# Kernel optimization log

Hardware: AMD Instinct MI355X
Metric: run time of the kernel (lower is better)

The kernel has to match this reference:

```python
import jax, jax.numpy as jnp
import numpy as np
from jax import lax

HIDDEN = 256      # hidden_dim
LATENT = 128      # latent_dim
VOCAB = 32000     # vocab_size
MAX_LEN = 64      # max_len (stack capacity guard, as in original)
MAX_STEPS = 128   # fixed step budget for the decode stack machine
N_NODES = 511     # complete binary tree, depth 9


def _linear_params(key, fan_in, fan_out):
    k1, k2 = jax.random.split(key)
    s = 1.0 / np.sqrt(fan_in)
    W = jax.random.uniform(k1, (fan_out, fan_in), minval=-s, maxval=s, dtype=jnp.float32)
    b = jax.random.uniform(k2, (fan_out,), minval=-s, maxval=s, dtype=jnp.float32)
    return W, b


def setup_inputs() -> dict:
    key = jax.random.key(0)
    ks = jax.random.split(key, 10)
    embed = jax.random.normal(ks[0], (VOCAB, HIDDEN), dtype=jnp.float32)
    Wpar, bpar = _linear_params(ks[1], 3 * HIDDEN, HIDDEN)
    Wmu, bmu = _linear_params(ks[2], HIDDEN, LATENT)
    Wlv, blv = _linear_params(ks[3], HIDDEN, LATENT)
    W1, b1 = _linear_params(ks[4], LATENT, HIDDEN)
    W2, b2 = _linear_params(ks[5], HIDDEN, HIDDEN + 1)
    Wl, bl = _linear_params(ks[6], HIDDEN, VOCAB)
    Wp, bp = _linear_params(ks[7], HIDDEN, 2 * LATENT + VOCAB)
    values = jax.random.randint(ks[8], (N_NODES,), 0, VOCAB)
    idx = np.arange(N_NODES)
    left = np.where(2 * idx + 1 < N_NODES, 2 * idx + 1, -1).astype(np.int32)
    right = np.where(2 * idx + 2 < N_NODES, 2 * idx + 2, -1).astype(np.int32)
    eps = jax.random.normal(ks[9], (LATENT,), dtype=jnp.float32)
    return dict(embed=embed, Wpar=Wpar, bpar=bpar, Wmu=Wmu, bmu=bmu,
                Wlv=Wlv, blv=blv, W1=W1, b1=b1, W2=W2, b2=b2,
                Wl=Wl, bl=bl, Wp=Wp, bp=bp, eps=eps,
                values=jnp.asarray(values), left=jnp.asarray(left), right=jnp.asarray(right))


def reference(embed, Wpar, bpar, Wmu, bmu, Wlv, blv, W1, b1, W2, b2,
              Wl, bl, Wp, bp, eps, values, left, right):
    # ---------- encode: bottom-up over tree stored as index arrays ----------
    emb = embed[values]  # [N, H], one gather for all node embeddings

    def enc_step(h, i):
        v = emb[i]
        li = jnp.maximum(left[i], 0)
        ri = jnp.maximum(right[i], 0)
        cat = jnp.concatenate([v, h[li], h[ri]])          # [3H]
        hp = cat @ Wpar.T + bpar                           # parent combine
        hi = jnp.where(left[i] < 0, v, hp)                 # leaf -> embedding
        return h.at[i].set(hi), None

    h0 = jnp.zeros((values.shape[0], HIDDEN), dtype=embed.dtype)
    # children have larger index than parents -> process in descending order
    h, _ = lax.scan(enc_step, h0, jnp.arange(values.shape[0] - 1, -1, -1))
    root = h[0]
    mu = root @ Wmu.T + bmu
    logvar = root @ Wlv.T + blv
    z = mu + eps * jnp.exp(0.5 * logvar)                   # reparameterize

    # ---------- decode: stack machine with fixed step budget ----------
    V, L = VOCAB, LATENT
    stack0 = jnp.zeros((MAX_LEN, L), dtype=z.dtype).at[0].set(z)
    out0 = jnp.zeros((MAX_STEPS, V), dtype=z.dtype)

    def dec_step(state, _):
        stack, sp, out, op = state
        active = sp > 0
        idx = jnp.maximum(sp - 1, 0)
        node = stack[idx]                                  # pop
        hmid = jax.nn.leaky_relu(node @ W1.T + b1, 0.2)
        co = hmid @ W2.T + b2                              # [H+1]; co[0] = gate
        is_parent = (co[0] > 0) & (sp - 1 <= MAX_LEN - 2) & active

        def parent_fn(_):
            dec = co[1:] @ Wp.T + bp                       # [V + 2L]
            value = dec[:V]
            ll = dec[V:V + L]
            rl = dec[V + L:]
            # original appends llatent then rlatent -> rlatent on top
            st = stack.at[idx].set(ll).at[idx + 1].set(rl)
            return value, st, sp + 1

        def leaf_fn(_):
            return co[1:] @ Wl.T + bl, stack, sp - 1

        value, st, nsp = lax.cond(is_parent, parent_fn, leaf_fn, None)
        m = active.astype(z.dtype)
        out = out.at[op].add(m * value)                    # rows written once
        stack = jnp.where(active, st, stack)
        sp = jnp.where(active, nsp, sp)
        op = op + active.astype(op.dtype)
        return (stack, sp, out, op), None

    init = (stack0, jnp.int32(1), out0, jnp.int32(0))
    (_, _, out, _), _ = lax.scan(dec_step, init, None, length=MAX_STEPS)
    return out, mu, logvar
```

## Files before the change

kernel.cpp:

```cpp
#include <hip/hip_runtime.h>

#define HID 256
#define LAT 128
#define VOC 32000
#define NSTEP 128

__global__ __launch_bounds__(512)
void prep_kernel(const float* __restrict__ Wp, const float* __restrict__ W2,
                 const float* __restrict__ b2, const float* __restrict__ bp,
                 const float* __restrict__ Wpar,
                 const float* __restrict__ Wmu, const float* __restrict__ Wlv,
                 float* __restrict__ Wcomb, float* __restrict__ bcomb,
                 float* __restrict__ Wq_par, float* __restrict__ Wq_mu,
                 float* __restrict__ Wq_lv, float* __restrict__ Wq_w2) {
    const int b = blockIdx.x;
    const int t = threadIdx.x;
    if (b < 256) {
        const int o = b;
        const int k = t & 255, jh = t >> 8;
        __shared__ float wpt_s[256];
        __shared__ float part_s[2][256];
        __shared__ float red_s[4];
        if (t < 256) wpt_s[t] = Wp[(size_t)(VOC + o) * HID + t];
        __syncthreads();
        float acc = 0.f;
#pragma unroll 8
        for (int j = 0; j < 128; j++)
            acc += wpt_s[jh * 128 + j] * W2[(size_t)(1 + jh * 128 + j) * HID + k];
        part_s[jh][k] = acc;
        if (t < 256) {
            float p = wpt_s[k] * b2[1 + k];
            p += __shfl_xor(p, 1);  p += __shfl_xor(p, 2);  p += __shfl_xor(p, 4);
            p += __shfl_xor(p, 8);  p += __shfl_xor(p, 16); p += __shfl_xor(p, 32);
            if ((k & 63) == 0) red_s[k >> 6] = p;
        }
        __syncthreads();
        if (t < 256) Wcomb[(size_t)o * HID + k] = part_s[0][k] + part_s[1][k];
        if (t == 0) bcomb[o] = bp[VOC + o] + red_s[0] + red_s[1] + red_s[2] + red_s[3];
    } else if (b < 352) {
        const int k4 = (b - 256) * 2 + (t >> 8);
        const int r = t & 255;
        ((float4*)Wq_par)[k4 * 256 + r] = *(const float4*)(Wpar + (size_t)r * 768 + 4 * k4);
    } else if (b < 384) {
        const int k4 = (b - 352) * 2 + (t >> 8);
        const int r = t & 127, sel = (t >> 7) & 1;
        const float* src = (sel ? Wlv : Wmu) + (size_t)r * HID + 4 * k4;
        ((float4*)(sel ? Wq_lv : Wq_mu))[k4 * 128 + r] = *(const float4*)src;
    } else {
        const int k4 = (b - 384) * 2 + (t >> 8);
        const int r = t & 255;
        ((float4*)Wq_w2)[k4 * 256 + r] = *(const float4*)(W2 + (size_t)(1 + r) * HID + 4 * k4);
    }
}

__global__ __launch_bounds__(1024)
void enc2(const float* __restrict__ embed, const int* __restrict__ values,
          const float* __restrict__ Wq, const float* __restrict__ bpar,
          float* __restrict__ h, int base) {
    const int i = base + blockIdx.x;
    const int t = threadIdx.x;
    const int o = t & 255;
    const int g = t >> 8;
    const int cid = g & 1, kh = g >> 1;
    __shared__ __align__(16) float cat[2][768];
    __shared__ float part[4][256];
    __shared__ __align__(16) float pcat[768];

    const int c0n = 2 * i + 1;
    for (int q = t; q < 1536; q += 1024) {
        const int cc = (q >= 768);
        const int e = q - cc * 768;
        const int node = c0n + cc;
        const int seg = e >> 8, idx = e & 255;
        float v;
        if (seg == 0) v = embed[(size_t)values[node] * HID + idx];
        else {
            const int ch = 2 * node + seg;
            v = (ch >= 255) ? embed[(size_t)values[ch] * HID + idx]
                            : h[(size_t)ch * HID + idx];
        }
        cat[cc][e] = v;
    }
    __syncthreads();
    {
        const float4* wq = (const float4*)Wq + o;
        const float4* c4 = (const float4*)cat[cid] + kh * 96;
        float s0 = 0.f, s1 = 0.f, s2 = 0.f, s3 = 0.f;
#pragma unroll 8
        for (int k4 = 0; k4 < 96; k4 += 4) {
            const float4 wa = wq[(size_t)(kh * 96 + k4) * 256];
            const float4 wb = wq[(size_t)(kh * 96 + k4 + 1) * 256];
            const float4 wc = wq[(size_t)(kh * 96 + k4 + 2) * 256];
            const float4 wd = wq[(size_t)(kh * 96 + k4 + 3) * 256];
            const float4 ca = c4[k4], cb = c4[k4 + 1], cx = c4[k4 + 2], cd = c4[k4 + 3];
            s0 = fmaf(wa.x, ca.x, s0); s0 = fmaf(wa.y, ca.y, s0);
            s0 = fmaf(wa.z, ca.z, s0); s0 = fmaf(wa.w, ca.w, s0);
            s1 = fmaf(wb.x, cb.x, s1); s1 = fmaf(wb.y, cb.y, s1);
            s1 = fmaf(wb.z, cb.z, s1); s1 = fmaf(wb.w, cb.w, s1);
            s2 = fmaf(wc.x, cx.x, s2); s2 = fmaf(wc.y, cx.y, s2);
            s2 = fmaf(wc.z, cx.z, s2); s2 = fmaf(wc.w, cx.w, s2);
            s3 = fmaf(wd.x, cd.x, s3); s3 = fmaf(wd.y, cd.y, s3);
            s3 = fmaf(wd.z, cd.z, s3); s3 = fmaf(wd.w, cd.w, s3);
        }
        part[g][o] = (s0 + s1) + (s2 + s3);
    }
    __syncthreads();
    if (t < 512) {
        const int c = t >> 8;
        pcat[256 + (c << 8) + o] = part[c][o] + part[c + 2][o] + bpar[o];
    } else if (t < 768) {
        const int idx = t & 255;
        pcat[idx] = embed[(size_t)values[i] * HID + idx];
    }
    __syncthreads();
    {
        const float4* wq = (const float4*)Wq + o;
        const float4* c4 = (const float4*)pcat + g * 48;
        float s0 = 0.f, s1 = 0.f, s2 = 0.f, s3 = 0.f;
#pragma unroll
        for (int k4 = 0; k4 < 48; k4 += 4) {
            const float4 wa = wq[(size_t)(g * 48 + k4) * 256];
            const float4 wb = wq[(size_t)(g * 48 + k4 + 1) * 256];
            const float4 wc = wq[(size_t)(g * 48 + k4 + 2) * 256];
            const float4 wd = wq[(size_t)(g * 48 + k4 + 3) * 256];
            const float4 ca = c4[k4], cb = c4[k4 + 1], cx = c4[k4 + 2], cd = c4[k4 + 3];
            s0 = fmaf(wa.x, ca.x, s0); s0 = fmaf(wa.y, ca.y, s0);
            s0 = fmaf(wa.z, ca.z, s0); s0 = fmaf(wa.w, ca.w, s0);
            s1 = fmaf(wb.x, cb.x, s1); s1 = fmaf(wb.y, cb.y, s1);
            s1 = fmaf(wb.z, cb.z, s1); s1 = fmaf(wb.w, cb.w, s1);
            s2 = fmaf(wc.x, cx.x, s2); s2 = fmaf(wc.y, cx.y, s2);
            s2 = fmaf(wc.z, cx.z, s2); s2 = fmaf(wc.w, cx.w, s2);
            s3 = fmaf(wd.x, cd.x, s3); s3 = fmaf(wd.w, cd.w, s3);
            s3 = fmaf(wd.y, cd.y, s3); s3 = fmaf(wd.z, cd.z, s3);
        }
        part[g][o] = (s0 + s1) + (s2 + s3);
    }
    __syncthreads();
    if (t < 256)
        h[(size_t)i * HID + t] = part[0][t] + part[1][t] + part[2][t] + part[3][t] + bpar[t];
}

__global__ __launch_bounds__(256)
void enc_lvl(const float* __restrict__ embed, const int* __restrict__ values,
             const float* __restrict__ Wq, const float* __restrict__ bpar,
             float* __restrict__ h, int first, int logS) {
    const int S = 1 << logS;
    const int R = 256 >> logS;
    const int node = first + (blockIdx.x >> logS);
    const int slice = blockIdx.x & (S - 1);
    const int t = threadIdx.x;
    const int rl = t & (R - 1);
    const int g = t >> (8 - logS);
    __shared__ __align__(16) float cat_s[768];
    __shared__ float part_s[256];

    for (int e = t; e < 768; e += 256) {
        const int seg = e >> 8, idx = e & 255;
        cat_s[e] = (seg == 0) ? embed[(size_t)values[node] * HID + idx]
                              : h[(size_t)(2 * node + seg) * HID + idx];
    }
    __syncthreads();

    const int r0 = slice * R;
    const int nk4 = 192 >> logS;
    const float4* wq = (const float4*)Wq + (size_t)(g * nk4) * 256 + r0 + rl;
    const float4* c4 = (const float4*)cat_s + g * nk4;
    float s0 = 0.f, s1 = 0.f, s2 = 0.f, s3 = 0.f;
    for (int k4 = 0; k4 < nk4; k4 += 4) {
        const float4 wa = wq[(size_t)(k4) * 256];
        const float4 wb = wq[(size_t)(k4 + 1) * 256];
        const float4 wc = wq[(size_t)(k4 + 2) * 256];
        const float4 wd = wq[(size_t)(k4 + 3) * 256];
        const float4 ca = c4[k4], cb = c4[k4 + 1], cx = c4[k4 + 2], cd = c4[k4 + 3];
        s0 = fmaf(wa.x, ca.x, s0); s0 = fmaf(wa.y, ca.y, s0);
        s0 = fmaf(wa.z, ca.z, s0); s0 = fmaf(wa.w, ca.w, s0);
        s1 = fmaf(wb.x, cb.x, s1); s1 = fmaf(wb.y, cb.y, s1);
        s1 = fmaf(wb.z, cb.z, s1); s1 = fmaf(wb.w, cb.w, s1);
        s2 = fmaf(wc.x, cx.x, s2); s2 = fmaf(wc.y, cx.y, s2);
        s2 = fmaf(wc.z, cx.z, s2); s2 = fmaf(wc.w, cx.w, s2);
        s3 = fmaf(wd.x, cd.x, s3); s3 = fmaf(wd.y, cd.y, s3);
        s3 = fmaf(wd.z, cd.z, s3); s3 = fmaf(wd.w, cd.w, s3);
    }
    part_s[t] = (s0 + s1) + (s2 + s3);
    __syncthreads();
    if (t < R) {
        float v = bpar[r0 + t];
        for (int g2 = 0; g2 < S; g2++) v += part_s[g2 * R + t];
        h[(size_t)node * HID + r0 + t] = v;
    }
}

__global__ __launch_bounds__(512, 2)
void recur_kernel(const float* W1, const float* b1,
                  const float* W2, const float* b2,
                  const float* Wcomb, const float* bcomb,
                  const float* h0,
                  const float* Wq_mu, const float* bmu,
                  const float* Wq_lv, const float* blv,
                  const float* eps, float* out,
                  float* Hrec, int* rowflag) {
    const int t = threadIdx.x;
    const int o = t >> 1;
    const int hk = t & 1;
    __shared__ __align__(16) float stack_s[64 * 128];
    __shared__ __align__(16) float hmid_s[256];

    float4 w1r[16];
#pragma unroll
    for (int j = 0; j < 16; j++)
        w1r[j] = *(const float4*)(W1 + (size_t)o * 128 + hk * 64 + 4 * j);
    float4 wcr[32];
#pragma unroll
    for (int j = 0; j < 32; j++)
        wcr[j] = *(const float4*)(Wcomb + (size_t)o * 256 + hk * 128 + 4 * j);

    const float b1o = b1[o];
    const float bco = bcomb[o];
    const float b20 = b2[0];
    const int l64 = t & 63;
    const float4 w2q = *(const float4*)(W2 + 4 * l64);

    if (t < 256) hmid_s[t] = h0[t];
    __syncthreads();
    {
        const int r = o & 127;
        const float4* wqh = (const float4*)(o < 128 ? Wq_mu : Wq_lv) + r;
        const float4* r4 = (const float4*)hmid_s + hk * 32;
        float s0 = 0.f, s1 = 0.f;
#pragma unroll
        for (int k4 = 0; k4 < 32; k4 += 2) {
            const float4 wa = wqh[(size_t)(hk * 32 + k4) * 128];
            const float4 wb = wqh[(size_t)(hk * 32 + k4 + 1) * 128];
            const float4 ca = r4[k4], cb = r4[k4 + 1];
            s0 = fmaf(wa.x, ca.x, s0); s0 = fmaf(wa.y, ca.y, s0);
            s0 = fmaf(wa.z, ca.z, s0); s0 = fmaf(wa.w, ca.w, s0);
            s1 = fmaf(wb.x, cb.x, s1); s1 = fmaf(wb.y, cb.y, s1);
            s1 = fmaf(wb.z, cb.z, s1); s1 = fmaf(wb.w, cb.w, s1);
        }
        float a = s0 + s1;
        a += __shfl_xor(a, 1);
        if (hk == 0) {
            const float v = a + (o < 128 ? bmu[r] : blv[r]);
            out[(size_t)NSTEP * VOC + o] = v;
            stack_s[128 + o] = v;
        }
    }
    __syncthreads();
    if (t < 128)
        stack_s[t] = stack_s[128 + t] + eps[t] * expf(0.5f * stack_s[256 + t]);

    int sp = 1, op = 0;
    unsigned long long pm0 = 0ULL, pm1 = 0ULL;
    __syncthreads();

    for (int step = 0; step < NSTEP; step++) {
        if (sp <= 0) break;
        const int idx = sp - 1;

        const float* np = stack_s + idx * 128 + hk * 64;
        float a0 = 0.f, a1 = 0.f;
#pragma unroll
        for (int j = 0; j < 16; j += 2) {
            const float4 v0 = *(const float4*)(np + 4 * j);
            const float4 v1 = *(const float4*)(np + 4 * j + 4);
            a0 = fmaf(w1r[j].x, v0.x, a0);     a0 = fmaf(w1r[j].y, v0.y, a0);
            a0 = fmaf(w1r[j].z, v0.z, a0);     a0 = fmaf(w1r[j].w, v0.w, a0);
            a1 = fmaf(w1r[j + 1].x, v1.x, a1); a1 = fmaf(w1r[j + 1].y, v1.y, a1);
            a1 = fmaf(w1r[j + 1].z, v1.z, a1); a1 = fmaf(w1r[j + 1].w, v1.w, a1);
        }
        float a = a0 + a1;
        a += __shfl_xor(a, 1);
        if (hk == 0) {
            float pre = a + b1o;
            pre = pre > 0.f ? pre : 0.2f * pre;
            hmid_s[o] = pre;
            Hrec[(size_t)op * HID + o] = pre;
        }
        __syncthreads();

        const float4 hq = *(const float4*)(hmid_s + 4 * l64);
        float c = w2q.x * hq.x + w2q.y * hq.y + w2q.z * hq.z + w2q.w * hq.w;
        c += __shfl_xor(c, 1);  c += __shfl_xor(c, 2);  c += __shfl_xor(c, 4);
        c += __shfl_xor(c, 8);  c += __shfl_xor(c, 16); c += __shfl_xor(c, 32);
        const bool par = ((c + b20) > 0.f) && (sp <= 63);

        if (par) {
            const float* hp = hmid_s + hk * 128;
            float s0 = 0.f, s1 = 0.f, s2 = 0.f, s3 = 0.f;
#pragma unroll
            for (int j = 0; j < 32; j += 4) {
                const float4 v0 = *(const float4*)(hp + 4 * j);
                const float4 v1 = *(const float4*)(hp + 4 * j + 4);
                const float4 v2 = *(const float4*)(hp + 4 * j + 8);
                const float4 v3 = *(const float4*)(hp + 4 * j + 12);
                s0 = fmaf(wcr[j].x, v0.x, s0);     s0 = fmaf(wcr[j].y, v0.y, s0);
                s0 = fmaf(wcr[j].z, v0.z, s0);     s0 = fmaf(wcr[j].w, v0.w, s0);
                s1 = fmaf(wcr[j + 1].x, v1.x, s1); s1 = fmaf(wcr[j + 1].y, v1.y, s1);
                s1 = fmaf(wcr[j + 1].z, v1.z, s1); s1 = fmaf(wcr[j + 1].w, v1.w, s1);
                s2 = fmaf(wcr[j + 2].x, v2.x, s2); s2 = fmaf(wcr[j + 2].y, v2.y, s2);
                s2 = fmaf(wcr[j + 2].z, v2.z, s2); s2 = fmaf(wcr[j + 2].w, v2.w, s2);
                s3 = fmaf(wcr[j + 3].x, v3.x, s3); s3 = fmaf(wcr[j + 3].y, v3.y, s3);
                s3 = fmaf(wcr[j + 3].z, v3.z, s3); s3 = fmaf(wcr[j + 3].w, v3.w, s3);
            }
            float s = (s0 + s1) + (s2 + s3);
            s += __shfl_xor(s, 1);
            if (hk == 0)
                stack_s[(idx + (o >> 7)) * 128 + (o & 127)] = s + bco;
            if (op < 64) pm0 |= (1ULL << op); else pm1 |= (1ULL << (op - 64));
            sp += 1;
        } else {
            sp -= 1;
        }
        op++;
        __syncthreads();
    }

    if (t < 128) {
        int f = -1;
        if (t < op) f = (t < 64) ? (int)((pm0 >> t) & 1) : (int)((pm1 >> (t - 64)) & 1);
        rowflag[t] = f;
    }
}

__global__ __launch_bounds__(256)
void co1_kernel(const float* __restrict__ Hrec, const float* __restrict__ Wq_w2,
                const float* __restrict__ b2, const int* __restrict__ rowflag,
                float* __restrict__ Co1, int* __restrict__ lists) {
    const int r = blockIdx.x;
    const int c = threadIdx.x;
    if (r == 128) {
        if (c == 0) {
            int nl = 0, np_ = 0, nz = 0;
            for (int q = 0; q < 128; q++) {
                const int f = rowflag[q];
                if (f == 0) lists[nl++] = q;
                else if (f == 1) lists[128 + np_++] = q;
                else lists[256 + nz++] = q;
            }
            lists[384] = nl; lists[385] = np_; lists[386] = nz;
        }
        return;
    }
    __shared__ __align__(16) float hs[256];
    hs[c] = Hrec[(size_t)r * HID + c];
    __syncthreads();
    const float4* wq = (const float4*)Wq_w2 + c;
    const float4* h4 = (const float4*)hs;
    float s0 = b2[1 + c], s1 = 0.f, s2 = 0.f, s3 = 0.f;
#pragma unroll 8
    for (int k4 = 0; k4 < 64; k4 += 4) {
        const float4 a0 = wq[(k4) * 256],     h0 = h4[k4];
        const float4 a1 = wq[(k4 + 1) * 256], h1 = h4[k4 + 1];
        const float4 a2 = wq[(k4 + 2) * 256], h2 = h4[k4 + 2];
        const float4 a3 = wq[(k4 + 3) * 256], h3 = h4[k4 + 3];
        s0 = fmaf(a0.x, h0.x, s0); s0 = fmaf(a0.y, h0.y, s0);
        s0 = fmaf(a0.z, h0.z, s0); s0 = fmaf(a0.w, h0.w, s0);
        s1 = fmaf(a1.x, h1.x, s1); s1 = fmaf(a1.y, h1.y, s1);
        s1 = fmaf(a1.z, h1.z, s1); s1 = fmaf(a1.w, h1.w, s1);
        s2 = fmaf(a2.x, h2.x, s2); s2 = fmaf(a2.y, h2.y, s2);
        s2 = fmaf(a2.z, h2.z, s2); s2 = fmaf(a2.w, h2.w, s2);
        s3 = fmaf(a3.x, h3.x, s3); s3 = fmaf(a3.y, h3.y, s3);
        s3 = fmaf(a3.z, h3.z, s3); s3 = fmaf(a3.w, h3.w, s3);
    }
    Co1[(size_t)r * HID + c] = (s0 + s1) + (s2 + s3);
}

__global__ __launch_bounds__(256, 2)
void value_kernel(const float* __restrict__ Co1, const int* __restrict__ lists,
                  const float* __restrict__ Wl, const float* __restrict__ bl,
                  const float* __restrict__ Wp, const float* __restrict__ bp,
                  float* __restrict__ out) {
    const int m = blockIdx.y;
    const int t = threadIdx.x;
    const int v = blockIdx.x * 128 + (t & 127);
    const int rh = t >> 7;
    const int n = lists[384 + m];
    const int* list = lists + m * 128;
    const float* Wx = m ? Wp : Wl;
    const float* bx = m ? bp : bl;
    const float bv = bx[v];
    const float4* w4 = (const float4*)(Wx + (size_t)v * HID);

    for (int rc = 0; rc < n; rc += 32) {
        const int nr = min(32, n - rc);
        float acc[16];
#pragma unroll
        for (int i = 0; i < 16; i++) acc[i] = 0.f;
        for (int kc = 0; kc < 4; kc++) {
            float4 w[16];
#pragma unroll
            for (int i = 0; i < 16; i++) w[i] = w4[kc * 16 + i];
#pragma unroll
            for (int aa = 0; aa < 16; aa++) {
                const int rr = 2 * aa + rh;
                if (rr < nr) {
                    const int row = __builtin_amdgcn_readfirstlane(list[rc + rr]);
                    const float* cp = Co1 + (size_t)row * HID + kc * 64;
                    float s0 = 0.f, s1 = 0.f, s2 = 0.f, s3 = 0.f;
#pragma unroll
                    for (int i = 0; i < 16; i += 4) {
                        const float4 c0 = *(const float4*)(cp + 4 * i);
                        const float4 c1 = *(const float4*)(cp + 4 * i + 4);
                        const float4 c2 = *(const float4*)(cp + 4 * i + 8);
                        const float4 c3 = *(const float4*)(cp + 4 * i + 12);
                        s0 = fmaf(w[i].x, c0.x, s0);     s0 = fmaf(w[i].y, c0.y, s0);
                        s0 = fmaf(w[i].z, c0.z, s0);     s0 = fmaf(w[i].w, c0.w, s0);
                        s1 = fmaf(w[i + 1].x, c1.x, s1); s1 = fmaf(w[i + 1].y, c1.y, s1);
                        s1 = fmaf(w[i + 1].z, c1.z, s1); s1 = fmaf(w[i + 1].w, c1.w, s1);
                        s2 = fmaf(w[i + 2].x, c2.x, s2); s2 = fmaf(w[i + 2].y, c2.y, s2);
                        s2 = fmaf(w[i + 2].z, c2.z, s2); s2 = fmaf(w[i + 2].w, c2.w, s2);
                        s3 = fmaf(w[i + 3].x, c3.x, s3); s3 = fmaf(w[i + 3].y, c3.y, s3);
                        s3 = fmaf(w[i + 3].z, c3.z, s3); s3 = fmaf(w[i + 3].w, c3.w, s3);
                    }
                    acc[aa] += (s0 + s1) + (s2 + s3);
                }
            }
        }
#pragma unroll
        for (int aa = 0; aa < 16; aa++) {
            const int rr = 2 * aa + rh;
            if (rr < nr) {
                const int row = __builtin_amdgcn_readfirstlane(list[rc + rr]);
                out[(size_t)row * VOC + v] = acc[aa] + bv;
            }
        }
    }
    if (m == 0 && rh == 0) {
        const int nz = lists[386];
        const int* zl = lists + 256;
        for (int i = 0; i < nz; i++)
            out[(size_t)zl[i] * VOC + v] = 0.f;
    }
}

extern "C" void kernel_launch(void* const* d_in, const int* in_sizes, int n_in,
                              void* d_out, int out_size, void* d_ws, size_t ws_size,
                              hipStream_t stream) {
    const float* embed = (const float*)d_in[0];
    const float* Wpar  = (const float*)d_in[1];
    const float* bpar  = (const float*)d_in[2];
    const float* Wmu   = (const float*)d_in[3];
    const float* bmu   = (const float*)d_in[4];
    const float* Wlv   = (const float*)d_in[5];
    const float* blv   = (const float*)d_in[6];
    const float* W1    = (const float*)d_in[7];
    const float* b1    = (const float*)d_in[8];
    const float* W2    = (const float*)d_in[9];
    const float* b2    = (const float*)d_in[10];
    const float* Wl    = (const float*)d_in[11];
    const float* bl    = (const float*)d_in[12];
    const float* Wp    = (const float*)d_in[13];
    const float* bp    = (const float*)d_in[14];
    const float* eps   = (const float*)d_in[15];
    const int*  values = (const int*)d_in[16];

    float* ws = (float*)d_ws;
    float* h       = ws;
    float* z       = ws + 65280;
    float* Wcomb   = ws + 65408;
    float* bcomb   = ws + 130944;
    float* Hrec    = ws + 131200;
    float* Co1     = ws + 163968;
    int*   rowflag = (int*)(ws + 196736);
    float* Wq_par  = ws + 196864;
    float* Wq_mu   = ws + 393472;
    float* Wq_lv   = ws + 426240;
    float* Wq_w2   = ws + 459008;
    int*   lists   = (int*)(ws + 524544);
    float* out = (float*)d_out;
    (void)z;

    prep_kernel<<<416, 512, 0, stream>>>(Wp, W2, b2, bp, Wpar, Wmu, Wlv,
                                         Wcomb, bcomb, Wq_par, Wq_mu, Wq_lv, Wq_w2);

    enc2<<<64, 1024, 0, stream>>>(embed, values, Wq_par, bpar, h, 63);
    enc_lvl<<<64, 256, 0, stream>>>(embed, values, Wq_par, bpar, h, 31, 1);
    enc_lvl<<<64, 256, 0, stream>>>(embed, values, Wq_par, bpar, h, 15, 2);
    enc_lvl<<<64, 256, 0, stream>>>(embed, values, Wq_par, bpar, h,  7, 3);
    enc_lvl<<<64, 256, 0, stream>>>(embed, values, Wq_par, bpar, h,  3, 4);
    enc_lvl<<<32, 256, 0, stream>>>(embed, values, Wq_par, bpar, h,  1, 4);
    enc_lvl<<<16, 256, 0, stream>>>(embed, values, Wq_par, bpar, h,  0, 4);

    recur_kernel<<<1, 512, 0, stream>>>(W1, b1, W2, b2, Wcomb, bcomb, h,
                                        Wq_mu, bmu, Wq_lv, blv, eps, out,
                                        Hrec, rowflag);

    co1_kernel<<<129, 256, 0, stream>>>(Hrec, Wq_w2, b2, rowflag, Co1, lists);
    value_kernel<<<dim3(250, 2), 256, 0, stream>>>(Co1, lists, Wl, bl, Wp, bp, out);
}
```

Before: 245.2 us.

## Fuse root encoder node into recurrence kernel and fold gate dot into hidden pass

Drops the last enc_lvl launch for the root node and computes the root combine inside recur_kernel from the embedding and child hidden states. Inside the decode loop, the gate dot product W2[0]·hmid is now computed from each thread's own activation with a wavefront reduction and a small shared partial array. That removes the separate post-barrier pass that re-read hmid from shared memory. The intent is to save one kernel launch and shorten each serial decode step, at the cost of a single block doing the 768-wide root matvec serially.

```diff
diff --git a/kernel.cpp b/kernel.cpp
--- a/kernel.cpp
+++ b/kernel.cpp
@@ -130,8 +130,8 @@
             s1 = fmaf(wb.z, cb.z, s1); s1 = fmaf(wb.w, cb.w, s1);
             s2 = fmaf(wc.x, cx.x, s2); s2 = fmaf(wc.y, cx.y, s2);
             s2 = fmaf(wc.z, cx.z, s2); s2 = fmaf(wc.w, cx.w, s2);
-            s3 = fmaf(wd.x, cd.x, s3); s3 = fmaf(wd.w, cd.w, s3);
-            s3 = fmaf(wd.y, cd.y, s3); s3 = fmaf(wd.z, cd.z, s3);
+            s3 = fmaf(wd.x, cd.x, s3); s3 = fmaf(wd.y, cd.y, s3);
+            s3 = fmaf(wd.z, cd.z, s3); s3 = fmaf(wd.w, cd.w, s3);
         }
         part[g][o] = (s0 + s1) + (s2 + s3);
     }
@@ -194,7 +194,9 @@
 void recur_kernel(const float* W1, const float* b1,
                   const float* W2, const float* b2,
                   const float* Wcomb, const float* bcomb,
-                  const float* h0,
+                  const float* embed, const int* values,
+                  const float* Wq_par, const float* bpar,
+                  const float* h,
                   const float* Wq_mu, const float* bmu,
                   const float* Wq_lv, const float* blv,
                   const float* eps, float* out,
@@ -204,6 +206,8 @@
     const int hk = t & 1;
     __shared__ __align__(16) float stack_s[64 * 128];
     __shared__ __align__(16) float hmid_s[256];
+    __shared__ __align__(16) float cat0_s[768];
+    __shared__ float c0part_s[8];
 
     float4 w1r[16];
 #pragma unroll
@@ -217,11 +221,40 @@
     const float b1o = b1[o];
     const float bco = bcomb[o];
     const float b20 = b2[0];
-    const int l64 = t & 63;
-    const float4 w2q = *(const float4*)(W2 + 4 * l64);
-
-    if (t < 256) hmid_s[t] = h0[t];
-    __syncthreads();
+    const float w2o = W2[o];
+
+    const int v0 = values[0];
+    for (int e = t; e < 768; e += 512) {
+        const int seg = e >> 8, idx = e & 255;
+        cat0_s[e] = (seg == 0) ? embed[(size_t)v0 * HID + idx]
+                               : h[(size_t)seg * HID + idx];
+    }
+    __syncthreads();
+    {
+        const float4* wq = (const float4*)Wq_par + (size_t)(hk * 96) * 256 + o;
+        const float4* c4 = (const float4*)cat0_s + hk * 96;
+        float s0 = 0.f, s1 = 0.f, s2 = 0.f, s3 = 0.f;
+        for (int k4 = 0; k4 < 96; k4 += 4) {
+            const float4 wa = wq[(size_t)(k4) * 256];
+            const float4 wb = wq[(size_t)(k4 + 1) * 256];
+            const float4 wc = wq[(size_t)(k4 + 2) * 256];
+            const float4 wd = wq[(size_t)(k4 + 3) * 256];
+            const float4 ca = c4[k4], cb = c4[k4 + 1], cx = c4[k4 + 2], cd = c4[k4 + 3];
+            s0 = fmaf(wa.x, ca.x, s0); s0 = fmaf(wa.y, ca.y, s0);
+            s0 = fmaf(wa.z, ca.z, s0); s0 = fmaf(wa.w, ca.w, s0);
+            s1 = fmaf(wb.x, cb.x, s1); s1 = fmaf(wb.y, cb.y, s1);
+            s1 = fmaf(wb.z, cb.z, s1); s1 = fmaf(wb.w, cb.w, s1);
+            s2 = fmaf(wc.x, cx.x, s2); s2 = fmaf(wc.y, cx.y, s2);
+            s2 = fmaf(wc.z, cx.z, s2); s2 = fmaf(wc.w, cx.w, s2);
+            s3 = fmaf(wd.x, cd.x, s3); s3 = fmaf(wd.y, cd.y, s3);
+            s3 = fmaf(wd.z, cd.z, s3); s3 = fmaf(wd.w, cd.w, s3);
+        }
+        float a = (s0 + s1) + (s2 + s3);
+        a += __shfl_xor(a, 1);
+        if (hk == 0) hmid_s[o] = a + bpar[o];
+    }
+    __syncthreads();
+
     {
         const int r = o & 127;
         const float4* wqh = (const float4*)(o < 128 ? Wq_mu : Wq_lv) + r;
@@ -240,7 +273,7 @@
         float a = s0 + s1;
         a += __shfl_xor(a, 1);
         if (hk == 0) {
-            const float v = a + (o < 128 ? bmu[r] : blv[r]);
+            const float v = a + (o < 128 ? bmu[o & 127] : blv[o & 127]);
             out[(size_t)NSTEP * VOC + o] = v;
             stack_s[128 + o] = v;
         }
@@ -261,46 +294,51 @@
         float a0 = 0.f, a1 = 0.f;
 #pragma unroll
         for (int j = 0; j < 16; j += 2) {
-            const float4 v0 = *(const float4*)(np + 4 * j);
-            const float4 v1 = *(const float4*)(np + 4 * j + 4);
-            a0 = fmaf(w1r[j].x, v0.x, a0);     a0 = fmaf(w1r[j].y, v0.y, a0);
-            a0 = fmaf(w1r[j].z, v0.z, a0);     a0 = fmaf(w1r[j].w, v0.w, a0);
-            a1 = fmaf(w1r[j + 1].x, v1.x, a1); a1 = fmaf(w1r[j + 1].y, v1.y, a1);
-            a1 = fmaf(w1r[j + 1].z, v1.z, a1); a1 = fmaf(w1r[j + 1].w, v1.w, a1);
+            const float4 v0r = *(const float4*)(np + 4 * j);
+            const float4 v1r = *(const float4*)(np + 4 * j + 4);
+            a0 = fmaf(w1r[j].x, v0r.x, a0);     a0 = fmaf(w1r[j].y, v0r.y, a0);
+            a0 = fmaf(w1r[j].z, v0r.z, a0);     a0 = fmaf(w1r[j].w, v0r.w, a0);
+            a1 = fmaf(w1r[j + 1].x, v1r.x, a1); a1 = fmaf(w1r[j + 1].y, v1r.y, a1);
+            a1 = fmaf(w1r[j + 1].z, v1r.z, a1); a1 = fmaf(w1r[j + 1].w, v1r.w, a1);
         }
         float a = a0 + a1;
         a += __shfl_xor(a, 1);
+
+        float act = a + b1o;
+        act = act > 0.f ? act : 0.2f * act;
+        float m = w2o * act;
+        m += __shfl_xor(m, 2);  m += __shfl_xor(m, 4);  m += __shfl_xor(m, 8);
+        m += __shfl_xor(m, 16); m += __shfl_xor(m, 32);
+        if ((t & 63) == 0) c0part_s[t >> 6] = m;
         if (hk == 0) {
-            float pre = a + b1o;
-            pre = pre > 0.f ? pre : 0.2f * pre;
-            hmid_s[o] = pre;
-            Hrec[(size_t)op * HID + o] = pre;
+            hmid_s[o] = act;
+            Hrec[(size_t)op * HID + o] = act;
         }
         __syncthreads();
 
-        const float4 hq = *(const float4*)(hmid_s + 4 * l64);
-        float c = w2q.x * hq.x + w2q.y * hq.y + w2q.z * hq.z + w2q.w * hq.w;
-        c += __shfl_xor(c, 1);  c += __shfl_xor(c, 2);  c += __shfl_xor(c, 4);
-        c += __shfl_xor(c, 8);  c += __shfl_xor(c, 16); c += __shfl_xor(c, 32);
-        const bool par = ((c + b20) > 0.f) && (sp <= 63);
+        const float4 q0 = ((const float4*)c0part_s)[0];
+        const float4 q1 = ((const float4*)c0part_s)[1];
+        const float c = ((q0.x + q0.y) + (q0.z + q0.w)) +
+                        ((q1.x + q1.y) + (q1.z + q1.w)) + b20;
+        const bool par = (c > 0.f) && (sp <= 63);
 
         if (par) {
             const float* hp = hmid_s + hk * 128;
             float s0 = 0.f, s1 = 0.f, s2 = 0.f, s3 = 0.f;
 #pragma unroll
             for (int j = 0; j < 32; j += 4) {
-                const float4 v0 = *(const float4*)(hp + 4 * j);
-                const float4 v1 = *(const float4*)(hp + 4 * j + 4);
-                const float4 v2 = *(const float4*)(hp + 4 * j + 8);
-                const float4 v3 = *(const float4*)(hp + 4 * j + 12);
-                s0 = fmaf(wcr[j].x, v0.x, s0);     s0 = fmaf(wcr[j].y, v0.y, s0);
-                s0 = fmaf(wcr[j].z, v0.z, s0);     s0 = fmaf(wcr[j].w, v0.w, s0);
-                s1 = fmaf(wcr[j + 1].x, v1.x, s1); s1 = fmaf(wcr[j + 1].y, v1.y, s1);
-                s1 = fmaf(wcr[j + 1].z, v1.z, s1); s1 = fmaf(wcr[j + 1].w, v1.w, s1);
-                s2 = fmaf(wcr[j + 2].x, v2.x, s2); s2 = fmaf(wcr[j + 2].y, v2.y, s2);
-                s2 = fmaf(wcr[j + 2].z, v2.z, s2); s2 = fmaf(wcr[j + 2].w, v2.w, s2);
-                s3 = fmaf(wcr[j + 3].x, v3.x, s3); s3 = fmaf(wcr[j + 3].y, v3.y, s3);
-                s3 = fmaf(wcr[j + 3].z, v3.z, s3); s3 = fmaf(wcr[j + 3].w, v3.w, s3);
+                const float4 v0r = *(const float4*)(hp + 4 * j);
+                const float4 v1r = *(const float4*)(hp + 4 * j + 4);
+                const float4 v2r = *(const float4*)(hp + 4 * j + 8);
+                const float4 v3r = *(const float4*)(hp + 4 * j + 12);
+                s0 = fmaf(wcr[j].x, v0r.x, s0);     s0 = fmaf(wcr[j].y, v0r.y, s0);
+                s0 = fmaf(wcr[j].z, v0r.z, s0);     s0 = fmaf(wcr[j].w, v0r.w, s0);
+                s1 = fmaf(wcr[j + 1].x, v1r.x, s1); s1 = fmaf(wcr[j + 1].y, v1r.y, s1);
+                s1 = fmaf(wcr[j + 1].z, v1r.z, s1); s1 = fmaf(wcr[j + 1].w, v1r.w, s1);
+                s2 = fmaf(wcr[j + 2].x, v2r.x, s2); s2 = fmaf(wcr[j + 2].y, v2r.y, s2);
+                s2 = fmaf(wcr[j + 2].z, v2r.z, s2); s2 = fmaf(wcr[j + 2].w, v2r.w, s2);
+                s3 = fmaf(wcr[j + 3].x, v3r.x, s3); s3 = fmaf(wcr[j + 3].y, v3r.y, s3);
+                s3 = fmaf(wcr[j + 3].w, v3r.w, s3); s3 = fmaf(wcr[j + 3].z, v3r.z, s3);
             }
             float s = (s0 + s1) + (s2 + s3);
             s += __shfl_xor(s, 1);
@@ -456,7 +494,6 @@
 
     float* ws = (float*)d_ws;
     float* h       = ws;
-    float* z       = ws + 65280;
     float* Wcomb   = ws + 65408;
     float* bcomb   = ws + 130944;
     float* Hrec    = ws + 131200;
@@ -468,7 +505,6 @@
     float* Wq_w2   = ws + 459008;
     int*   lists   = (int*)(ws + 524544);
     float* out = (float*)d_out;
-    (void)z;
 
     prep_kernel<<<416, 512, 0, stream>>>(Wp, W2, b2, bp, Wpar, Wmu, Wlv,
                                          Wcomb, bcomb, Wq_par, Wq_mu, Wq_lv, Wq_w2);
@@ -479,9 +515,9 @@
     enc_lvl<<<64, 256, 0, stream>>>(embed, values, Wq_par, bpar, h,  7, 3);
     enc_lvl<<<64, 256, 0, stream>>>(embed, values, Wq_par, bpar, h,  3, 4);
     enc_lvl<<<32, 256, 0, stream>>>(embed, values, Wq_par, bpar, h,  1, 4);
-    enc_lvl<<<16, 256, 0, stream>>>(embed, values, Wq_par, bpar, h,  0, 4);
-
-    recur_kernel<<<1, 512, 0, stream>>>(W1, b1, W2, b2, Wcomb, bcomb, h,
+
+    recur_kernel<<<1, 512, 0, stream>>>(W1, b1, W2, b2, Wcomb, bcomb,
+                                        embed, values, Wq_par, bpar, h,
                                         Wq_mu, bmu, Wq_lv, blv, eps, out,
                                         Hrec, rowflag);
 
```

After: 254.9 us. +4.0%, slower.
